# Kernel tuning notes

Hardware: AMD Instinct MI355X
Metric: run time of the kernel (lower is better)

The kernel has to match this reference:

```python
import jax, jax.numpy as jnp
import numpy as np

HEADS = 8
DIM_HEAD = 64


def setup_inputs() -> dict:
    key = jax.random.key(0)
    ks = jax.random.split(key, 5)
    B, N, C, coor = 2, 2048, 256, 3
    dim_inner = HEADS * DIM_HEAD  # 512
    # weight scale 1/16 ~ 1/sqrt(256) keeps softmax logits in a sane range
    w_scale = 1.0 / 16.0
    return {
        "x": jax.random.normal(ks[0], (B, N, C, coor), dtype=jnp.float32),
        "Wq": jax.random.normal(ks[1], (dim_inner, C), dtype=jnp.float32) * w_scale,
        "Wk": jax.random.normal(ks[2], (dim_inner, C), dtype=jnp.float32) * w_scale,
        "Wv": jax.random.normal(ks[3], (dim_inner, C), dtype=jnp.float32) * w_scale,
        "Wo": jax.random.normal(ks[4], (C, dim_inner), dtype=jnp.float32) * w_scale,
    }


def _split_heads(t, B, N, coor):
    # b n (h d) c -> b h n (d c)
    t = t.reshape(B, N, HEADS, DIM_HEAD, coor)
    t = t.transpose(0, 2, 1, 3, 4)
    return t.reshape(B, HEADS, N, DIM_HEAD * coor)


def reference(x, Wq, Wk, Wv, Wo):
    B, N, C, coor = x.shape
    # VNLinear: einsum('... i c, o i -> ... o c')
    q = jnp.einsum('bnic,oi->bnoc', x, Wq)
    k = jnp.einsum('bnic,oi->bnoc', x, Wk)
    v = jnp.einsum('bnic,oi->bnoc', x, Wv)
    q = _split_heads(q, B, N, coor)  # (B, H, N, d*c)
    k = _split_heads(k, B, N, coor)
    v = _split_heads(v, B, N, coor)
    scale = (DIM_HEAD * coor) ** -0.5
    sim = jnp.einsum('bhie,bhje->bhij', q, k) * scale  # (B, H, N, N)
    attn = jax.nn.softmax(sim, axis=-1)
    out = jnp.einsum('bhij,bhje->bhie', attn, v)  # (B, H, N, d*c)
    # b h n (d c) -> b n (h d) c
    out = out.reshape(B, HEADS, N, DIM_HEAD, coor).transpose(0, 2, 1, 3, 4)
    out = out.reshape(B, N, HEADS * DIM_HEAD, coor)
    # to_out VNLinear
    return jnp.einsum('bnic,oi->bnoc', out, Wo)  # (B, N, C, 3)
```

## Files before the change

kernel.cpp:

```cpp
#include <hip/hip_runtime.h>

#define HEADS 8
#define DH 64
#define CO 3
#define E 192
#define NSEQ 2048
#define BATCH 2
#define CIN 256
#define DINNER 512
#define NTOK 4096
#define BHTOT 16

typedef __attribute__((ext_vector_type(8))) short bf16x8;
typedef __attribute__((ext_vector_type(4))) short bf16x4;
typedef __attribute__((ext_vector_type(4))) float f32x4;
typedef __attribute__((ext_vector_type(4))) float float4v;

static __device__ inline short f2bf(float f) {
  union { float f; unsigned u; } v; v.f = f;
  unsigned r = (v.u + 0x7FFFu + ((v.u >> 16) & 1u)) >> 16;
  return (short)r;
}

static __device__ inline float bf2f(short s) {
  union { unsigned u; float f; } a;
  a.u = ((unsigned)(unsigned short)s) << 16;
  return a.f;
}

static __device__ inline void load_lds16(const short* g, short* l) {
  __builtin_amdgcn_global_load_lds(
      (const __attribute__((address_space(1))) void*)g,
      (__attribute__((address_space(3))) void*)l, 16, 0, 0);
}


__global__ __launch_bounds__(256) void prep(const float* __restrict__ x,
                                            const float* __restrict__ Wq,
                                            const float* __restrict__ Wk,
                                            const float* __restrict__ Wv,
                                            const float* __restrict__ Wo,
                                            short* __restrict__ xcp,
                                            short* __restrict__ wqkvp,
                                            short* __restrict__ wop) {
  int tid = threadIdx.x;
  if (blockIdx.x < 256) {
    __shared__ short st[12288];
    int mt = blockIdx.x;
    const float* xb = x + (size_t)mt * 12288;
#pragma unroll
    for (int r = 0; r < 12; r++) {
      int idx4 = r * 256 + tid;
      float4v v = *(const float4v*)(xb + idx4 * 4);
#pragma unroll
      for (int e = 0; e < 4; e++) {
        int fp = idx4 * 4 + e;
        int ti = fp / 3, c = fp - ti * 3;
        int tl = ti >> 8, i = ti & 255;
        int ks = i >> 5, qd = (i >> 3) & 3, j = i & 7;
        st[c * 4096 + ks * 512 + (qd * 16 + tl) * 8 + j] = f2bf(v[e]);
      }
    }
    __syncthreads();
    short* dst = xcp;
#pragma unroll
    for (int rep = 0; rep < 6; rep++) {
      int g = rep * 256 + tid;
      int c = g >> 9, rem = g & 511;
      *(bf16x8*)(dst + ((size_t)(c * 256 + mt) * 8) * 512 + rem * 8) =
          *(const bf16x8*)&st[c * 4096 + rem * 8];
    }
    return;
  }
  int idx = (blockIdx.x - 256) * 256 + tid;
  const float qscale = 0.07216878364870323f * 1.4426950408889634f;
  if (idx < 1536 * 256) {
    int o = idx >> 8, i = idx & 255;
    float v;
    if (o < 512) v = Wq[idx] * qscale;
    else if (o < 1024) v = Wk[idx - 512 * 256];
    else v = Wv[idx - 1024 * 256];
    int nt = o >> 4, ln = o & 15, ks = i >> 5, qd = (i >> 3) & 3, j = i & 7;
    wqkvp[((size_t)(nt * 8 + ks)) * 512 + (qd * 16 + ln) * 8 + j] = f2bf(v);
  } else {
    int j0 = idx - 1536 * 256;
    if (j0 < 256 * 512) {
      int o2 = j0 >> 9, i = j0 & 511;
      int nt = o2 >> 4, ln = o2 & 15, ks = i >> 5, qd = (i >> 3) & 3, j = i & 7;
      wop[((size_t)(nt * 16 + ks)) * 512 + (qd * 16 + ln) * 8 + j] = f2bf(Wo[j0]);
    }
  }
}

__global__ __launch_bounds__(256, 4) void qkv_gemm(const short* __restrict__ xcp,
                                                   const short* __restrict__ wqkvp,
                                                   short* __restrict__ qp,
                                                   short* __restrict__ kp,
                                                   short* __restrict__ vp) {
  __shared__ __align__(16) short pool[9216];
  int c = blockIdx.z, ntb = blockIdx.x, mtb = blockIdx.y;
  int tid = threadIdx.x, wave = tid >> 6, lane = tid & 63;
  int ln = lane & 15, quad = lane >> 4;
  int wm = wave >> 1, wn = wave & 1;

  const short* gA = xcp + ((size_t)(c * 256 + mtb * 8) * 8) * 512;

  f32x4 acc[4][2] = {};
#pragma unroll
  for (int i = 0; i < 2; i++) {
    int q = tid + 256 * i, mf = q >> 6, l = q & 63;
    load_lds16(gA + (size_t)(mf * 8) * 512 + l * 8, pool + q * 8);
  }
  for (int ks = 0; ks < 8; ks++) {
    int b = ks & 1;
    __syncthreads();
    if (ks < 7) {
#pragma unroll
      for (int i = 0; i < 2; i++) {
        int q = tid + 256 * i, mf = q >> 6, l = q & 63;
        load_lds16(gA + (size_t)(mf * 8 + ks + 1) * 512 + l * 8,
                   pool + (b ^ 1) * 4096 + q * 8);
      }
    }
    const short* As = pool + b * 4096;
    bf16x8 af[4], bfr[2];
#pragma unroll
    for (int j = 0; j < 2; j++)
      bfr[j] = *(const bf16x8*)(wqkvp +
          (size_t)((ntb * 4 + wn * 2 + j) * 8 + ks) * 512 + lane * 8);
#pragma unroll
    for (int i = 0; i < 4; i++) af[i] = *(const bf16x8*)&As[(wm * 4 + i) * 512 + lane * 8];
#pragma unroll
    for (int i = 0; i < 4; i++)
#pragma unroll
      for (int j = 0; j < 2; j++)
        acc[i][j] = __builtin_amdgcn_mfma_f32_16x16x32_bf16(af[i], bfr[j], acc[i][j], 0, 0, 0);
  }

  int mat = ntb >> 3;
  int h = ntb & 7;
  int b0 = mtb >> 4;
  int bhx = b0 * 8 + h;
  if (mat < 2) {
    __syncthreads();
    short* tp = pool;
#pragma unroll
    for (int i = 0; i < 4; i++)
#pragma unroll
      for (int j = 0; j < 2; j++)
#pragma unroll
        for (int jj = 0; jj < 4; jj++)
          tp[(wm * 64 + i * 16 + quad * 4 + jj) * 72 + wn * 32 + j * 16 + ln] =
              f2bf(acc[i][j][jj]);
    __syncthreads();
    short* dst = (mat == 0) ? qp : kp;
#pragma unroll
    for (int rep = 0; rep < 4; rep++) {
      int gi = rep * 256 + tid;
      int l2 = gi & 15, qd = (gi >> 4) & 3, nf2 = (gi >> 6) & 3,
          esp = (gi >> 8) & 1, kt2 = (gi >> 9) & 1;
      int tl = kt2 * 64 + nf2 * 16 + l2;
      bf16x8 val = *(const bf16x8*)&tp[tl * 72 + esp * 32 + qd * 8];
      int kt = (mtb * 2 + kt2) & 31;
      int es = c * 2 + esp;
      size_t off = (((size_t)((bhx * 32 + kt) * 24) + es * 4 + nf2) * 64 +
                    (size_t)(qd * 16 + l2)) * 8;
      *(bf16x8*)(dst + off) = val;
    }
  } else {
#pragma unroll
    for (int i = 0; i < 4; i++) {
      int kt = (mtb * 2 + wm) & 31;
      int ks2 = (i >> 1) & 1;
      int qd2 = (i * 2 + (quad >> 1)) & 3;
#pragma unroll
      for (int j = 0; j < 2; j++) {
        int ef = c * 4 + wn * 2 + j;
        size_t off = ((size_t)((bhx * 32 + kt) * 24 + ks2 * 12 + ef)) * 512 +
                     (qd2 * 16 + ln) * 8 + (quad & 1) * 4;
        bf16x4 val = { f2bf(acc[i][j][0]), f2bf(acc[i][j][1]),
                       f2bf(acc[i][j][2]), f2bf(acc[i][j][3]) };
        *(bf16x4*)(vp + off) = val;
      }
    }
  }
}

__global__ __launch_bounds__(256, 2) void attn(const short* __restrict__ qp,
                                               const short* __restrict__ kp,
                                               const short* __restrict__ vp,
                                               short* __restrict__ opart,
                                               float* __restrict__ lpart) {
  __shared__ __align__(16) short pool[29696];
  int pair = blockIdx.x, qt = blockIdx.y;
  int bh = pair & 15, kh = pair >> 4;
  int tid = threadIdx.x, wave = tid >> 6, lane = tid & 63;
  int ln = lane & 15, quad = lane >> 4;
  short* Pl = pool + 24576;

  bf16x8 qf[2][6];
#pragma unroll
  for (int rg = 0; rg < 2; rg++) {
    int fi = wave * 2 + rg;
    const short* qb = qp +
        ((size_t)(bh * 32 + qt * 2 + (fi >> 2)) * 24 + (fi & 3)) * 512 + lane * 8;
#pragma unroll
    for (int es = 0; es < 6; es++) qf[rg][es] = *(const bf16x8*)(qb + es * 2048);
  }

  float l_r[2] = {0.f, 0.f};
  f32x4 acc[2][12] = {};
  const short* gKb = kp + (size_t)(bh * 32 + kh * 16) * 12288;
  const short* gVb = vp + (size_t)(bh * 32 + kh * 16) * 12288;

  auto stage = [&](int k32, int buf) {
    const short* g64K = gKb + (size_t)(k32 >> 1) * 12288;
    const short* g64V = gVb + (size_t)(k32 >> 1) * 12288;
    int half = k32 & 1;
    short* Kd = pool + buf * 6144;
    short* Vd = pool + 12288 + buf * 6144;
#pragma unroll
    for (int i = 0; i < 3; i++) {
      int q = i * 256 + tid;
      int f = q >> 6, l = q & 63;
      int es = f >> 1, nfl = f & 1;
      load_lds16(g64K + (size_t)(es * 4 + half * 2 + nfl) * 512 + l * 8, Kd + q * 8);
      load_lds16(g64V + (size_t)(half * 12 + f) * 512 + l * 8, Vd + q * 8);
    }
  };

  stage(0, 0);
  for (int kt = 0; kt < 32; kt++) {
    int b = kt & 1;
    __syncthreads();
    if (kt < 31) stage(kt + 1, b ^ 1);
    const short* Kl = pool + b * 6144;
    const short* Vl = pool + 12288 + b * 6144;

    f32x4 s[2][2] = {};
#pragma unroll
    for (int es = 0; es < 6; es++) {
#pragma unroll
      for (int nfl = 0; nfl < 2; nfl++) {
        bf16x8 kf = *(const bf16x8*)&Kl[(es * 2 + nfl) * 512 + lane * 8];
        s[0][nfl] = __builtin_amdgcn_mfma_f32_16x16x32_bf16(kf, qf[0][es], s[0][nfl], 0, 0, 0);
        s[1][nfl] = __builtin_amdgcn_mfma_f32_16x16x32_bf16(kf, qf[1][es], s[1][nfl], 0, 0, 0);
      }
    }

#pragma unroll
    for (int rg = 0; rg < 2; rg++)
#pragma unroll
      for (int nfl = 0; nfl < 2; nfl++) {
        bf16x4 pk4;
#pragma unroll
        for (int jj = 0; jj < 4; jj++) {
          float p = __builtin_amdgcn_exp2f(s[rg][nfl][jj]);
          union { float f; unsigned u; } v; v.f = p;
          pk4[jj] = (short)((v.u + 0x8000u) >> 16);
          l_r[rg] += p;
        }
        *(bf16x4*)&Pl[((wave * 2 + rg) * 16 + ln) * 40 + nfl * 16 + quad * 4] = pk4;
      }

    bf16x8 pa[2];
#pragma unroll
    for (int rg = 0; rg < 2; rg++)
      pa[rg] = *(const bf16x8*)&Pl[((wave * 2 + rg) * 16 + ln) * 40 + quad * 8];

#pragma unroll
    for (int ef = 0; ef < 12; ef++) {
      bf16x8 v0 = *(const bf16x8*)&Vl[ef * 512 + lane * 8];
      acc[0][ef] = __builtin_amdgcn_mfma_f32_16x16x32_bf16(pa[0], v0, acc[0][ef], 0, 0, 0);
      acc[1][ef] = __builtin_amdgcn_mfma_f32_16x16x32_bf16(pa[1], v0, acc[1][ef], 0, 0, 0);
    }
  }

#pragma unroll
  for (int rg = 0; rg < 2; rg++) {
    l_r[rg] += __shfl_xor(l_r[rg], 16, 64);
    l_r[rg] += __shfl_xor(l_r[rg], 32, 64);
  }

  __syncthreads();
  short* tp = pool;
#pragma unroll
  for (int rg = 0; rg < 2; rg++)
#pragma unroll
    for (int jj = 0; jj < 4; jj++) {
      int row = (wave * 2 + rg) * 16 + quad * 4 + jj;
#pragma unroll
      for (int ef = 0; ef < 12; ef++)
        tp[row * 200 + ef * 16 + ln] = f2bf(acc[rg][ef][jj]);
    }
  __syncthreads();
  const size_t obase = ((size_t)(kh * 16 + bh) * 2048 + qt * 128) * 192;
#pragma unroll
  for (int rep = 0; rep < 12; rep++) {
    int gi = rep * 256 + tid;
    int row = gi / 24, c8 = gi - row * 24;
    *(bf16x8*)(opart + obase + (size_t)row * 192 + c8 * 8) =
        *(const bf16x8*)&tp[row * 200 + c8 * 8];
  }
  int lb = (kh * 16 + bh) * 2048 + qt * 128;
  if (quad == 0) {
#pragma unroll
    for (int rg = 0; rg < 2; rg++)
      lpart[lb + (wave * 2 + rg) * 16 + ln] = l_r[rg];
  }
}

__global__ __launch_bounds__(256) void out_gemm(const short* __restrict__ opart,
                                                const float* __restrict__ lpart,
                                                const short* __restrict__ wop,
                                                float* __restrict__ out) {
  __shared__ __align__(16) float pool_f[12352];
  short* Al = (short*)pool_f;
  int mtb = blockIdx.x;
  int tid = threadIdx.x, wave = tid >> 6, lane = tid & 63;
  int ln = lane & 15, quad = lane >> 4;
  const size_t HSTR = (size_t)16 * 2048 * 192;

#pragma unroll
  for (int rep = 0; rep < 12; rep++) {
    int g = rep * 256 + tid;
    int c = g >> 10, inner = g & 1023;
    int d8 = inner & 7, h = (inner >> 3) & 7, row16 = inner >> 6;
    int t = mtb * 16 + row16, b = t >> 11, n = t & 2047;
    int bh = b * 8 + h;
    size_t src = ((size_t)bh * 2048 + n) * 192 + c * 64 + d8 * 8;
    bf16x8 o1 = *(const bf16x8*)(opart + src);
    bf16x8 o2 = *(const bf16x8*)(opart + HSTR + src);
    float l = lpart[bh * 2048 + n] + lpart[32768 + bh * 2048 + n];
    float inv = 1.f / l;
    bf16x8 r;
#pragma unroll
    for (int j = 0; j < 8; j++) r[j] = f2bf((bf2f(o1[j]) + bf2f(o2[j])) * inv);
    int ks = h * 2 + (d8 >> 2), qd = d8 & 3;
    *(bf16x8*)&Al[c * 8192 + ks * 512 + (qd * 16 + row16) * 8] = r;
  }
  __syncthreads();

  f32x4 acc[3][4] = {};
  for (int ks = 0; ks < 16; ks++) {
    bf16x8 af[3];
#pragma unroll
    for (int c = 0; c < 3; c++) af[c] = *(const bf16x8*)&Al[c * 8192 + ks * 512 + lane * 8];
#pragma unroll
    for (int jf = 0; jf < 4; jf++) {
      int nt = wave * 4 + jf;
      bf16x8 bfr = *(const bf16x8*)(wop + (size_t)(nt * 16 + ks) * 512 + lane * 8);
#pragma unroll
      for (int c = 0; c < 3; c++)
        acc[c][jf] = __builtin_amdgcn_mfma_f32_16x16x32_bf16(af[c], bfr, acc[c][jf], 0, 0, 0);
    }
  }
  __syncthreads();
#pragma unroll
  for (int c = 0; c < 3; c++)
#pragma unroll
    for (int jf = 0; jf < 4; jf++) {
      int o2 = (wave * 4 + jf) * 16 + ln;
#pragma unroll
      for (int jj = 0; jj < 4; jj++)
        pool_f[(quad * 4 + jj) * 772 + o2 * 3 + c] = acc[c][jf][jj];
    }
  __syncthreads();
  float* ob = out + (size_t)mtb * 12288;
#pragma unroll
  for (int rep = 0; rep < 12; rep++) {
    int idx = rep * 256 + tid;
    int row = idx / 192, col4 = idx - row * 192;
    *(float4v*)(ob + row * 768 + col4 * 4) =
        *(const float4v*)(pool_f + row * 772 + col4 * 4);
  }
}

extern "C" void kernel_launch(void* const* d_in, const int* in_sizes, int n_in,
                              void* d_out, int out_size, void* d_ws, size_t ws_size,
                              hipStream_t stream) {
  const float* x  = (const float*)d_in[0];
  const float* Wq = (const float*)d_in[1];
  const float* Wk = (const float*)d_in[2];
  const float* Wv = (const float*)d_in[3];
  const float* Wo = (const float*)d_in[4];
  float* out = (float*)d_out;

  short* ws    = (short*)d_ws;
  short* xcp   = ws;
  short* wqkvp = xcp + 3 * NTOK * CIN;
  short* wop   = wqkvp + 1536 * 256;
  short* qp    = wop + 256 * 512;
  short* kp    = qp + (size_t)BHTOT * NSEQ * E;
  short* vp    = kp + (size_t)BHTOT * NSEQ * E;
  short* opart = vp + (size_t)BHTOT * NSEQ * E;
  float* lpart = (float*)xcp;

  prep<<<2304, 256, 0, stream>>>(x, Wq, Wk, Wv, Wo, xcp, wqkvp, wop);
  qkv_gemm<<<dim3(24, 32, 3), 256, 0, stream>>>(xcp, wqkvp, qp, kp, vp);
  attn<<<dim3(32, 16), 256, 0, stream>>>(qp, kp, vp, opart, lpart);
  out_gemm<<<256, 256, 0, stream>>>(opart, lpart, wop, out);
}
```

Baseline: 158.6 us.

## Software-pipeline PV matmul one tile behind and build P fragments in registers

The attention loop now issues the P·V MFMAs for the previous key tile right after the current QK MFMAs, so the exp and pack work overlaps with matrix work. The P tile no longer goes through LDS: it is packed with v_cvt_pk_bf16_f32 and redistributed across lanes with permlane32_swap, and the V projection writer permutes its quad layout to match. K and V staging are split so V is loaded one iteration later, s_setprio raises wave priority around the MFMA block, and LDS use shrinks. This adds register pressure from the carried pa fragments and an extra epilogue, and it relies on the changed V layout lining up exactly with the swapped lane order.

```diff
diff --git a/kernel.cpp b/kernel.cpp
--- a/kernel.cpp
+++ b/kernel.cpp
@@ -168,16 +168,17 @@
       *(bf16x8*)(dst + off) = val;
     }
   } else {
+    int q2 = quad ^ (((quad ^ (quad >> 1)) & 1) * 3);
 #pragma unroll
     for (int i = 0; i < 4; i++) {
       int kt = (mtb * 2 + wm) & 31;
       int ks2 = (i >> 1) & 1;
-      int qd2 = (i * 2 + (quad >> 1)) & 3;
+      int qd2 = (i * 2 + (q2 >> 1)) & 3;
 #pragma unroll
       for (int j = 0; j < 2; j++) {
         int ef = c * 4 + wn * 2 + j;
         size_t off = ((size_t)((bhx * 32 + kt) * 24 + ks2 * 12 + ef)) * 512 +
-                     (qd2 * 16 + ln) * 8 + (quad & 1) * 4;
+                     (qd2 * 16 + ln) * 8 + (q2 & 1) * 4;
         bf16x4 val = { f2bf(acc[i][j][0]), f2bf(acc[i][j][1]),
                        f2bf(acc[i][j][2]), f2bf(acc[i][j][3]) };
         *(bf16x4*)(vp + off) = val;
@@ -191,12 +192,11 @@
                                                const short* __restrict__ vp,
                                                short* __restrict__ opart,
                                                float* __restrict__ lpart) {
-  __shared__ __align__(16) short pool[29696];
+  __shared__ __align__(16) short pool[25600];
   int pair = blockIdx.x, qt = blockIdx.y;
   int bh = pair & 15, kh = pair >> 4;
   int tid = threadIdx.x, wave = tid >> 6, lane = tid & 63;
   int ln = lane & 15, quad = lane >> 4;
-  short* Pl = pool + 24576;
 
   bf16x8 qf[2][6];
 #pragma unroll
@@ -210,33 +210,44 @@
 
   float l_r[2] = {0.f, 0.f};
   f32x4 acc[2][12] = {};
+  bf16x8 pa[2] = {};
   const short* gKb = kp + (size_t)(bh * 32 + kh * 16) * 12288;
   const short* gVb = vp + (size_t)(bh * 32 + kh * 16) * 12288;
 
-  auto stage = [&](int k32, int buf) {
-    const short* g64K = gKb + (size_t)(k32 >> 1) * 12288;
-    const short* g64V = gVb + (size_t)(k32 >> 1) * 12288;
+  auto stage_k = [&](int k32) {
+    const short* g64 = gKb + (size_t)(k32 >> 1) * 12288;
     int half = k32 & 1;
-    short* Kd = pool + buf * 6144;
-    short* Vd = pool + 12288 + buf * 6144;
+    short* Kd = pool + (k32 & 1) * 6144;
 #pragma unroll
     for (int i = 0; i < 3; i++) {
       int q = i * 256 + tid;
       int f = q >> 6, l = q & 63;
       int es = f >> 1, nfl = f & 1;
-      load_lds16(g64K + (size_t)(es * 4 + half * 2 + nfl) * 512 + l * 8, Kd + q * 8);
-      load_lds16(g64V + (size_t)(half * 12 + f) * 512 + l * 8, Vd + q * 8);
+      load_lds16(g64 + (size_t)(es * 4 + half * 2 + nfl) * 512 + l * 8, Kd + q * 8);
     }
   };
-
-  stage(0, 0);
+  auto stage_v = [&](int k32) {
+    const short* g64 = gVb + (size_t)(k32 >> 1) * 12288;
+    int half = k32 & 1;
+    short* Vd = pool + 12288 + (k32 & 1) * 6144;
+#pragma unroll
+    for (int i = 0; i < 3; i++) {
+      int q = i * 256 + tid;
+      int f = q >> 6, l = q & 63;
+      load_lds16(g64 + (size_t)(half * 12 + f) * 512 + l * 8, Vd + q * 8);
+    }
+  };
+
+  stage_k(0);
   for (int kt = 0; kt < 32; kt++) {
     int b = kt & 1;
     __syncthreads();
-    if (kt < 31) stage(kt + 1, b ^ 1);
+    if (kt < 31) stage_k(kt + 1);
+    stage_v(kt);
     const short* Kl = pool + b * 6144;
-    const short* Vl = pool + 12288 + b * 6144;
-
+    const short* Vl = pool + 12288 + ((kt - 1) & 1) * 6144;
+
+    __builtin_amdgcn_s_setprio(1);
     f32x4 s[2][2] = {};
 #pragma unroll
     for (int es = 0; es < 6; es++) {
@@ -247,27 +258,43 @@
         s[1][nfl] = __builtin_amdgcn_mfma_f32_16x16x32_bf16(kf, qf[1][es], s[1][nfl], 0, 0, 0);
       }
     }
-
-#pragma unroll
-    for (int rg = 0; rg < 2; rg++)
-#pragma unroll
-      for (int nfl = 0; nfl < 2; nfl++) {
-        bf16x4 pk4;
-#pragma unroll
-        for (int jj = 0; jj < 4; jj++) {
-          float p = __builtin_amdgcn_exp2f(s[rg][nfl][jj]);
-          union { float f; unsigned u; } v; v.f = p;
-          pk4[jj] = (short)((v.u + 0x8000u) >> 16);
-          l_r[rg] += p;
-        }
-        *(bf16x4*)&Pl[((wave * 2 + rg) * 16 + ln) * 40 + nfl * 16 + quad * 4] = pk4;
-      }
-
-    bf16x8 pa[2];
-#pragma unroll
-    for (int rg = 0; rg < 2; rg++)
-      pa[rg] = *(const bf16x8*)&Pl[((wave * 2 + rg) * 16 + ln) * 40 + quad * 8];
-
+    if (kt > 0) {
+#pragma unroll
+      for (int ef = 0; ef < 12; ef++) {
+        bf16x8 v0 = *(const bf16x8*)&Vl[ef * 512 + lane * 8];
+        acc[0][ef] = __builtin_amdgcn_mfma_f32_16x16x32_bf16(pa[0], v0, acc[0][ef], 0, 0, 0);
+        acc[1][ef] = __builtin_amdgcn_mfma_f32_16x16x32_bf16(pa[1], v0, acc[1][ef], 0, 0, 0);
+      }
+    }
+    __builtin_amdgcn_s_setprio(0);
+
+#pragma unroll
+    for (int rg = 0; rg < 2; rg++) {
+      float p0[4], p1[4];
+#pragma unroll
+      for (int jj = 0; jj < 4; jj++) {
+        float e0 = __builtin_amdgcn_exp2f(s[rg][0][jj]);
+        float e1 = __builtin_amdgcn_exp2f(s[rg][1][jj]);
+        p0[jj] = e0; p1[jj] = e1;
+        l_r[rg] += e0;
+        l_r[rg] += e1;
+      }
+      unsigned a0, a1, b0, b1;
+      asm("v_cvt_pk_bf16_f32 %0, %1, %2" : "=v"(a0) : "v"(p0[0]), "v"(p0[1]));
+      asm("v_cvt_pk_bf16_f32 %0, %1, %2" : "=v"(a1) : "v"(p0[2]), "v"(p0[3]));
+      asm("v_cvt_pk_bf16_f32 %0, %1, %2" : "=v"(b0) : "v"(p1[0]), "v"(p1[1]));
+      asm("v_cvt_pk_bf16_f32 %0, %1, %2" : "=v"(b1) : "v"(p1[2]), "v"(p1[3]));
+      auto r0 = __builtin_amdgcn_permlane32_swap(a0, b0, false, false);
+      auto r1 = __builtin_amdgcn_permlane32_swap(a1, b1, false, false);
+      union { unsigned u[4]; bf16x8 v; } pk;
+      pk.u[0] = r0[0]; pk.u[1] = r1[0]; pk.u[2] = r0[1]; pk.u[3] = r1[1];
+      pa[rg] = pk.v;
+    }
+  }
+
+  __syncthreads();
+  {
+    const short* Vl = pool + 12288 + 6144;
 #pragma unroll
     for (int ef = 0; ef < 12; ef++) {
       bf16x8 v0 = *(const bf16x8*)&Vl[ef * 512 + lane * 8];
```

After: 154.8 us. 2.3% less time.
